# Kernel optimization log

Measured on AMD Instinct MI355X. Metric: run time of the kernel, lower is better.

Reference implementation:

```python
import jax, jax.numpy as jnp
import numpy as np

DIM = 768
HEADS = 12


def setup_inputs() -> dict:
    key = jax.random.key(0)
    ks = jax.random.split(key, 8)
    B, N, C = 4, 1024, DIM
    x = jax.random.normal(ks[0], (B, N, C), dtype=jnp.float32)
    mask = jax.random.normal(ks[1], (B, 1, N, N), dtype=jnp.float32)
    weight = jax.random.uniform(ks[2], (B, N), dtype=jnp.float32)
    s = 1.0 / np.sqrt(C)
    qkv_w = jax.random.normal(ks[3], (3 * C, C), dtype=jnp.float32) * s
    mu_w = jax.random.normal(ks[4], (C, C // 2), dtype=jnp.float32) * s
    mu_b = jnp.zeros((C,), dtype=jnp.float32)
    ls_w = jax.random.normal(ks[5], (C, C // 2), dtype=jnp.float32) * s
    ls_b = jnp.zeros((C,), dtype=jnp.float32)
    return {"x": x, "mask": mask, "weight": weight, "qkv_w": qkv_w,
            "mu_w": mu_w, "mu_b": mu_b, "ls_w": ls_w, "ls_b": ls_b}


def reference(x, mask, weight, qkv_w, mu_w, mu_b, ls_w, ls_b):
    B, N, C = x.shape
    H = HEADS
    Dh = C // H
    # NOTE: module uses head_dim = dim * num_heads for the scale (quirk, kept faithful)
    scale = (C * H) ** (-0.5)
    qkv = (x @ qkv_w.T).reshape(B, N, 3, H, Dh).transpose(2, 0, 3, 1, 4)  # [3,B,H,N,Dh]
    q, k, v = qkv[0], qkv[1], qkv[2]
    attn = jnp.einsum('bhnd,bhmd->bhnm', q, k) * scale + mask  # [B,H,N,N]
    attn = jax.nn.softmax(attn, axis=-1)
    # weight: [B,N] broadcast over heads and queries (key axis)
    w = weight[:, None, None, :] + 1e-10
    attn = attn * w
    attn = attn / attn.sum(axis=-1, keepdims=True)
    out = jnp.einsum('bhnm,bhmd->bhnd', attn, v)          # [B,H,N,Dh]
    out = out.transpose(0, 2, 1, 3).reshape(B, N, C)      # [B,N,C]
    mu_in = out[:, :, :C // 2]
    ls_in = out[:, :, C // 2:]
    mu = mu_in @ mu_w.T + mu_b
    logsigma = ls_in @ ls_w.T + ls_b
    return (mu, logsigma, attn)
```

## Files before the change

kernel.cpp:

```cpp
#include <hip/hip_runtime.h>
#include <hip/hip_bf16.h>

typedef __attribute__((ext_vector_type(8))) short short8;
typedef __attribute__((ext_vector_type(4))) float f32x4;
typedef __attribute__((ext_vector_type(4))) unsigned short u16x4;

#define NB 4
#define NN 1024
#define NC 768
#define NH 12
#define TC 2304

#define OFF_XB   0ul
#define OFF_WQ   6291456ul
#define OFF_WMU  (OFF_WQ + 3538944ul)
#define OFF_WLS  (OFF_WMU + 589824ul)
#define OFF_QKVB (OFF_WLS + 589824ul)
#define OFF_V3   (OFF_QKVB + 18874368ul)
#define OFF_OUTB (OFF_V3 + 6291456ul)

__device__ __forceinline__ unsigned short f2bf(float f) {
    unsigned int u = __float_as_uint(f);
    u = (u + 0x7FFFu + ((u >> 16) & 1u)) >> 16;
    return (unsigned short)u;
}

__device__ __forceinline__ void gload_lds16(const unsigned short* g, unsigned short* l) {
    __builtin_amdgcn_global_load_lds(
        (const __attribute__((address_space(1))) unsigned int*)g,
        (__attribute__((address_space(3))) unsigned int*)l, 16, 0, 0);
}

__device__ __forceinline__ void gload16(short8& dst, const unsigned short* p) {
    asm volatile("global_load_dwordx4 %0, %1, off" : "=v"(dst) : "v"(p));
}
__device__ __forceinline__ void gloadf4(f32x4& dst, const float* p) {
    asm volatile("global_load_dwordx4 %0, %1, off" : "=v"(dst) : "v"(p));
}
#define WAITV(N) do { asm volatile("s_waitcnt vmcnt(" #N ")" ::: "memory"); \
                      __builtin_amdgcn_sched_barrier(0); } while (0)
#define SBAR()   __builtin_amdgcn_sched_barrier(0)

__global__ void cast_all(const float* __restrict__ x, const float* __restrict__ qkv_w,
                         const float* __restrict__ mu_w, const float* __restrict__ ls_w,
                         unsigned short* __restrict__ dst) {
    int i = blockIdx.x * blockDim.x + threadIdx.x;
    const float* src; int off;
    if (i < 786432)            { src = x;     off = i; }
    else if (i < 1228800)      { src = qkv_w; off = i - 786432; }
    else if (i < 1302528)      { src = mu_w;  off = i - 1228800; }
    else                       { src = ls_w;  off = i - 1302528; }
    f32x4 v = ((const f32x4*)src)[off];
    u16x4 o;
#pragma unroll
    for (int j = 0; j < 4; ++j) o[j] = f2bf(v[j]);
    ((u16x4*)dst)[i] = o;
}

template <int EPI>
__device__ __forceinline__ void gemm_body(
    unsigned short* As, unsigned short* Bs,
    const unsigned short* __restrict__ A, const unsigned short* __restrict__ Bm,
    int K, int lda, int ldb, void* __restrict__ Cout, int ldc,
    const float* __restrict__ bias, int row0, int col0)
{
    const int t = threadIdx.x;
    const int lane = t & 63;
    const int wv = t >> 6;
    const int wm = wv >> 1, wn = wv & 1;
    const int li = lane & 15;
    const int koff = (lane >> 4) * 8;

    f32x4 acc[4][4] = {};

    const int tr = t >> 2;
    const int tc = (t & 3) * 8;
    const unsigned short* ag = A + (size_t)(row0 + tr) * lda + tc;
    const unsigned short* bg = Bm + (size_t)(col0 + tr) * ldb + tc;

    for (int kt = 0; kt < K; kt += 32) {
        gload_lds16(ag,            As + t * 8);
        gload_lds16(ag + 64 * lda, As + 2048 + t * 8);
        gload_lds16(bg,            Bs + t * 8);
        gload_lds16(bg + 64 * ldb, Bs + 2048 + t * 8);
        ag += 32; bg += 32;
        __syncthreads();
        short8 af[4], bf[4];
#pragma unroll
        for (int m = 0; m < 4; ++m)
            af[m] = *(const short8*)&As[(wm * 64 + m * 16 + li) * 32 + koff];
#pragma unroll
        for (int n = 0; n < 4; ++n)
            bf[n] = *(const short8*)&Bs[(wn * 64 + n * 16 + li) * 32 + koff];
#pragma unroll
        for (int m = 0; m < 4; ++m)
#pragma unroll
            for (int n = 0; n < 4; ++n)
                acc[m][n] = __builtin_amdgcn_mfma_f32_16x16x32_bf16(af[m], bf[n], acc[m][n], 0, 0, 0);
        __syncthreads();
    }

#pragma unroll
    for (int m = 0; m < 4; ++m) {
        const int row = row0 + wm * 64 + m * 16 + (lane >> 4) * 4;
#pragma unroll
        for (int n = 0; n < 4; ++n) {
            const int col = col0 + wn * 64 + n * 16 + li;
#pragma unroll
            for (int r = 0; r < 4; ++r) {
                if (EPI == 0) {
                    ((unsigned short*)Cout)[(size_t)(row + r) * ldc + col] = f2bf(acc[m][n][r]);
                } else {
                    ((float*)Cout)[(size_t)(row + r) * ldc + col] = acc[m][n][r] + bias[col];
                }
            }
        }
    }
}

__global__ __launch_bounds__(256, 2) void gemm_qkv(
    const unsigned short* __restrict__ A, const unsigned short* __restrict__ Bm,
    unsigned short* __restrict__ C)
{
    __shared__ unsigned short As[128 * 32];
    __shared__ unsigned short Bs[128 * 32];
    const int bid = blockIdx.y * gridDim.x + blockIdx.x;
    const int nwg = gridDim.x * gridDim.y;
    const int swz = (bid & 7) * (nwg >> 3) + (bid >> 3);
    const int row0 = (swz / gridDim.x) * 128;
    const int col0 = (swz % gridDim.x) * 128;
    gemm_body<0>(As, Bs, A, Bm, NC, NC, NC, C, TC, nullptr, row0, col0);
}

__global__ __launch_bounds__(256, 2) void gemm_heads(
    const unsigned short* __restrict__ outb,
    const unsigned short* __restrict__ wmu, const unsigned short* __restrict__ wls,
    const float* __restrict__ mu_b, const float* __restrict__ ls_b,
    float* __restrict__ out_mu, float* __restrict__ out_ls)
{
    __shared__ unsigned short As[128 * 32];
    __shared__ unsigned short Bs[128 * 32];
    const int bid = blockIdx.y * gridDim.x + blockIdx.x;
    const int nwg = gridDim.x * gridDim.y;
    const int swz = (bid & 7) * (nwg >> 3) + (bid >> 3);
    const int row0 = (swz / gridDim.x) * 128;
    const int col0 = (swz % gridDim.x) * 128;
    const int z = blockIdx.z;
    gemm_body<1>(As, Bs, outb + (z ? 384 : 0), z ? wls : wmu, 384, NC, 384,
                 z ? (void*)out_ls : (void*)out_mu, NC, z ? ls_b : mu_b, row0, col0);
}

__global__ __launch_bounds__(256, 4) void pack_kv(
    const unsigned short* __restrict__ qkvb, unsigned short* __restrict__ kp,
    unsigned short* __restrict__ v3)
{
    __shared__ unsigned short tile[64][65];
    const int t = threadIdx.x;
    const int bh = blockIdx.y;
    const int b = bh / NH, h = bh % NH;
    const int m0 = blockIdx.x * 64;
#pragma unroll
    for (int i = 0; i < 2; ++i) {
        int lin = i * 256 + t;
        int mr = lin >> 3;
        int dr = (lin & 7) * 8;
        short8 v = *(const short8*)(qkvb + (size_t)(b * NN + m0 + mr) * TC + 768 + h * 64 + dr);
        int dbyte = (dr * 2) ^ ((mr & 7) << 4);
        *(short8*)(kp + (size_t)(bh * NN + m0 + mr) * 64 + (dbyte >> 1)) = v;
    }
#pragma unroll
    for (int i = 0; i < 2; ++i) {
        int lin = i * 256 + t;
        int mr = lin >> 3;
        int dr = (lin & 7) * 8;
        short8 v = *(const short8*)(qkvb + (size_t)(b * NN + m0 + mr) * TC + 1536 + h * 64 + dr);
#pragma unroll
        for (int j = 0; j < 8; ++j) tile[mr][dr + j] = (unsigned short)v[j];
    }
    __syncthreads();
#pragma unroll
    for (int i = 0; i < 2; ++i) {
        int lin = i * 256 + t;
        int dw = lin >> 3;
        int mw = (lin & 7) * 8;
        short8 v;
#pragma unroll
        for (int j = 0; j < 8; ++j) v[j] = (short)tile[mw + j][dw];
        int kt = (m0 + mw) >> 5;
        int mm = mw & 31;
        *(short8*)(v3 + ((size_t)(bh * 32 + kt) * 64 + dw) * 32 + mm) = v;
    }
}

__global__ __launch_bounds__(256, 3) void attn_kernel(
    const unsigned short* __restrict__ qkvb, const unsigned short* __restrict__ kp,
    const unsigned short* __restrict__ v3, const float* __restrict__ mask,
    const float* __restrict__ weight, float* __restrict__ attn_out,
    unsigned short* __restrict__ outb)
{
    __shared__ char smem[33024];
    __shared__ float red_max[4][16];
    __shared__ float red_sum[4][16];

    const int t = threadIdx.x;
    const int lane = t & 63;
    const int wv = t >> 6;
    const int li = lane & 15;
    const int g = lane >> 4;
    const int koff = g * 8;
    const int bh = blockIdx.y;
    const int b = bh / NH, h = bh % NH;
    const int n0 = blockIdx.x * 16;
    const int cb = wv * 256;

    unsigned short* kw = (unsigned short*)smem + wv * 4096;
    const unsigned short* kps = kp + (size_t)bh * 65536 + cb * 64;
    const float* mrow = mask + (size_t)b * NN * NN + (size_t)(n0 + li) * NN + cb + g * 4;

    f32x4 w4;
    gloadf4(w4, weight + b * NN + cb + lane * 4);
    const unsigned short* qp = qkvb + (size_t)(b * NN + n0 + li) * TC + h * 64 + koff;
    short8 qf0, qf1;
    gload16(qf0, qp);
    gload16(qf1, qp + 32);

    f32x4 acc[16];
    f32x4 mk[2][2];

#define KISSUE(c) do {                                                        \
        const unsigned short* ks_ = kps + (c) * 2048;                         \
        unsigned short* kd_ = kw + ((c) & 1) * 2048;                          \
        gload_lds16(ks_ + 0 * 512 + lane * 8, kd_ + 0 * 512 + lane * 8);      \
        gload_lds16(ks_ + 1 * 512 + lane * 8, kd_ + 1 * 512 + lane * 8);      \
        gload_lds16(ks_ + 2 * 512 + lane * 8, kd_ + 2 * 512 + lane * 8);      \
        gload_lds16(ks_ + 3 * 512 + lane * 8, kd_ + 3 * 512 + lane * 8);      \
        gloadf4(mk[(c) & 1][0], mrow + ((c) * 2 + 0) * 16);                   \
        gloadf4(mk[(c) & 1][1], mrow + ((c) * 2 + 1) * 16);                   \
    } while (0)

#define KSTEP(c) do {                                                         \
        const unsigned short* kb_ = kw + ((c) & 1) * 2048;                    \
        const int swz_ = (li & 7) << 4;                                       \
        _Pragma("unroll")                                                     \
        for (int s = 0; s < 2; ++s) {                                         \
            const int keyb_ = (s * 16 + li) * 64;                             \
            short8 kf0 = *(const short8*)&kb_[keyb_ + (((g * 16) ^ swz_) >> 1)];        \
            short8 kf1 = *(const short8*)&kb_[keyb_ + (((64 + g * 16) ^ swz_) >> 1)];   \
            f32x4 ci = mk[(c) & 1][s] * 96.0f;                                \
            ci = __builtin_amdgcn_mfma_f32_16x16x32_bf16(kf0, qf0, ci, 0, 0, 0); \
            ci = __builtin_amdgcn_mfma_f32_16x16x32_bf16(kf1, qf1, ci, 0, 0, 0); \
            acc[(c) * 2 + s] = ci;                                            \
        }                                                                     \
    } while (0)

    KISSUE(0); KISSUE(1);
    WAITV(6);  KSTEP(0); SBAR(); KISSUE(2);
    WAITV(6);  KSTEP(1); SBAR(); KISSUE(3);
    WAITV(6);  KSTEP(2); SBAR(); KISSUE(4);
    WAITV(6);  KSTEP(3); SBAR(); KISSUE(5);
    WAITV(6);  KSTEP(4); SBAR(); KISSUE(6);
    WAITV(6);  KSTEP(5); SBAR(); KISSUE(7);
    WAITV(6);  KSTEP(6);
    WAITV(0);  KSTEP(7);
#undef KISSUE
#undef KSTEP

    const float scale = 1.0f / 96.0f;
    float rmax = -1e30f;
#pragma unroll
    for (int cf = 0; cf < 16; ++cf) {
#pragma unroll
        for (int r = 0; r < 4; ++r) rmax = fmaxf(rmax, acc[cf][r]);
    }
    rmax = fmaxf(rmax, __shfl_xor(rmax, 16, 64));
    rmax = fmaxf(rmax, __shfl_xor(rmax, 32, 64));
    if (lane < 16) red_max[wv][lane] = rmax;
    __syncthreads();
    rmax = fmaxf(fmaxf(red_max[0][li], red_max[1][li]),
                 fmaxf(red_max[2][li], red_max[3][li])) * scale;

    unsigned short (*P)[1032] = (unsigned short(*)[1032])smem;
    float rsum = 0.f;
#pragma unroll
    for (int cf = 0; cf < 16; ++cf) {
        f32x4 wcf;
#pragma unroll
        for (int r = 0; r < 4; ++r) wcf[r] = __shfl(w4[r], cf * 4 + g, 64);
        u16x4 pb;
#pragma unroll
        for (int r = 0; r < 4; ++r) {
            float p = __expf(acc[cf][r] * scale - rmax) * (wcf[r] + 1e-10f);
            acc[cf][r] = p;
            rsum += p;
            pb[r] = f2bf(p);
        }
        *(u16x4*)&P[li][cb + cf * 16 + g * 4] = pb;
    }
    rsum += __shfl_xor(rsum, 16, 64);
    rsum += __shfl_xor(rsum, 32, 64);
    if (lane < 16) red_sum[wv][lane] = rsum;
    __syncthreads();

    f32x4 o = {};
    const unsigned short* v3s = v3 + (size_t)bh * 65536 + wv * 512 + li * 32 + g * 8;
    short8 vA[8], vB[8];
#define VISSUE(c, vb2) do {                                                   \
        _Pragma("unroll")                                                     \
        for (int j = 0; j < 8; ++j) gload16(vb2[j], v3s + ((c) * 8 + j) * 2048); \
    } while (0)
#define VCOMP(c, vb2) do {                                                    \
        _Pragma("unroll")                                                     \
        for (int j = 0; j < 8; ++j) {                                         \
            short8 pa = *(const short8*)&P[li][((c) * 8 + j) * 32 + koff];    \
            o = __builtin_amdgcn_mfma_f32_16x16x32_bf16(pa, vb2[j], o, 0, 0, 0); \
        }                                                                     \
    } while (0)
    VISSUE(0, vA);
    VISSUE(1, vB);
    WAITV(8);  VCOMP(0, vA); SBAR(); VISSUE(2, vA);
    WAITV(8);  VCOMP(1, vB); SBAR(); VISSUE(3, vB);
    WAITV(8);  VCOMP(2, vA);
    WAITV(0);  VCOMP(3, vB);
#undef VISSUE
#undef VCOMP

    const float rinv = 1.0f / (red_sum[0][li] + red_sum[1][li]
                             + red_sum[2][li] + red_sum[3][li]);
    const int dcol = h * 64 + wv * 16 + li;
#pragma unroll
    for (int r = 0; r < 4; ++r) {
        const int row = g * 4 + r;
        const float rv = 1.0f / (red_sum[0][row] + red_sum[1][row]
                               + red_sum[2][row] + red_sum[3][row]);
        outb[(size_t)(b * NN + n0 + row) * NC + dcol] = f2bf(o[r] * rv);
    }

    float* arow = attn_out + (size_t)bh * NN * NN + (size_t)(n0 + li) * NN + cb + g * 4;
#pragma unroll
    for (int cf = 0; cf < 16; ++cf) {
        f32x4 a4;
#pragma unroll
        for (int r = 0; r < 4; ++r) a4[r] = acc[cf][r] * rinv;
        *(f32x4*)(arow + cf * 16) = a4;
    }
}

extern "C" void kernel_launch(void* const* d_in, const int* in_sizes, int n_in,
                              void* d_out, int out_size, void* d_ws, size_t ws_size,
                              hipStream_t stream) {
    const float* x      = (const float*)d_in[0];
    const float* mask   = (const float*)d_in[1];
    const float* weight = (const float*)d_in[2];
    const float* qkv_w  = (const float*)d_in[3];
    const float* mu_w   = (const float*)d_in[4];
    const float* mu_b   = (const float*)d_in[5];
    const float* ls_w   = (const float*)d_in[6];
    const float* ls_b   = (const float*)d_in[7];

    char* ws = (char*)d_ws;
    unsigned short* xb   = (unsigned short*)(ws + OFF_XB);
    unsigned short* kp   = (unsigned short*)(ws + OFF_XB);
    unsigned short* wq   = (unsigned short*)(ws + OFF_WQ);
    unsigned short* wmu  = (unsigned short*)(ws + OFF_WMU);
    unsigned short* wls  = (unsigned short*)(ws + OFF_WLS);
    unsigned short* qkvb = (unsigned short*)(ws + OFF_QKVB);
    unsigned short* v3   = (unsigned short*)(ws + OFF_V3);
    unsigned short* outb = (unsigned short*)(ws + OFF_OUTB);

    float* out_mu   = (float*)d_out;
    float* out_ls   = out_mu + 3145728;
    float* out_attn = out_mu + 6291456;

    cast_all<<<5376, 256, 0, stream>>>(x, qkv_w, mu_w, ls_w, xb);

    gemm_qkv<<<dim3(TC / 128, 4096 / 128), 256, 0, stream>>>(xb, wq, qkvb);

    pack_kv<<<dim3(NN / 64, NB * NH), 256, 0, stream>>>(qkvb, kp, v3);

    attn_kernel<<<dim3(NN / 16, NB * NH), 256, 0, stream>>>(
        qkvb, kp, v3, mask, weight, out_attn, outb);

    gemm_heads<<<dim3(NC / 128, 4096 / 128, 2), 256, 0, stream>>>(
        outb, wmu, wls, mu_b, ls_b, out_mu, out_ls);
}
```

Baseline: 161.5 us.

## Remap attention blocks per XCD for mask reuse and triple-buffer K tiles

Replaces the 2D grid with a 1D grid whose block index is decoded so that blocks on the same XCD share a (batch, query-tile) across all heads, letting the mask rows be reused in that XCD's L2. Also deepens the K/mask prefetch pipeline from double to triple buffering, raising LDS per block to 48KB and adding mask registers. This trades extra LDS and registers, which could hurt occupancy, for better memory latency hiding and cache hit rate.

```diff
diff --git a/kernel.cpp b/kernel.cpp
--- a/kernel.cpp
+++ b/kernel.cpp
@@ -198,7 +198,7 @@
     const float* __restrict__ weight, float* __restrict__ attn_out,
     unsigned short* __restrict__ outb)
 {
-    __shared__ char smem[33024];
+    __shared__ char smem[49152];
     __shared__ float red_max[4][16];
     __shared__ float red_sum[4][16];
 
@@ -208,12 +208,17 @@
     const int li = lane & 15;
     const int g = lane >> 4;
     const int koff = g * 8;
-    const int bh = blockIdx.y;
-    const int b = bh / NH, h = bh % NH;
-    const int n0 = blockIdx.x * 16;
+
+    const int bid = blockIdx.x;
+    const int xcd = bid & 7, slot = bid >> 3;
+    const int h = slot % 12, gh = slot / 12;
+    const int g12 = gh * 8 + xcd;
+    const int b = g12 >> 6, nt = g12 & 63;
+    const int n0 = nt * 16;
+    const int bh = b * NH + h;
     const int cb = wv * 256;
 
-    unsigned short* kw = (unsigned short*)smem + wv * 4096;
+    unsigned short* kw = (unsigned short*)smem + wv * 6144;
     const unsigned short* kps = kp + (size_t)bh * 65536 + cb * 64;
     const float* mrow = mask + (size_t)b * NN * NN + (size_t)(n0 + li) * NN + cb + g * 4;
 
@@ -225,42 +230,42 @@
     gload16(qf1, qp + 32);
 
     f32x4 acc[16];
-    f32x4 mk[2][2];
+    f32x4 mk[3][2];
 
 #define KISSUE(c) do {                                                        \
         const unsigned short* ks_ = kps + (c) * 2048;                         \
-        unsigned short* kd_ = kw + ((c) & 1) * 2048;                          \
+        unsigned short* kd_ = kw + ((c) % 3) * 2048;                          \
         gload_lds16(ks_ + 0 * 512 + lane * 8, kd_ + 0 * 512 + lane * 8);      \
         gload_lds16(ks_ + 1 * 512 + lane * 8, kd_ + 1 * 512 + lane * 8);      \
         gload_lds16(ks_ + 2 * 512 + lane * 8, kd_ + 2 * 512 + lane * 8);      \
         gload_lds16(ks_ + 3 * 512 + lane * 8, kd_ + 3 * 512 + lane * 8);      \
-        gloadf4(mk[(c) & 1][0], mrow + ((c) * 2 + 0) * 16);                   \
-        gloadf4(mk[(c) & 1][1], mrow + ((c) * 2 + 1) * 16);                   \
+        gloadf4(mk[(c) % 3][0], mrow + ((c) * 2 + 0) * 16);                   \
+        gloadf4(mk[(c) % 3][1], mrow + ((c) * 2 + 1) * 16);                   \
     } while (0)
 
 #define KSTEP(c) do {                                                         \
-        const unsigned short* kb_ = kw + ((c) & 1) * 2048;                    \
+        const unsigned short* kb_ = kw + ((c) % 3) * 2048;                    \
         const int swz_ = (li & 7) << 4;                                       \
         _Pragma("unroll")                                                     \
         for (int s = 0; s < 2; ++s) {                                         \
             const int keyb_ = (s * 16 + li) * 64;                             \
             short8 kf0 = *(const short8*)&kb_[keyb_ + (((g * 16) ^ swz_) >> 1)];        \
             short8 kf1 = *(const short8*)&kb_[keyb_ + (((64 + g * 16) ^ swz_) >> 1)];   \
-            f32x4 ci = mk[(c) & 1][s] * 96.0f;                                \
+            f32x4 ci = mk[(c) % 3][s] * 96.0f;                                \
             ci = __builtin_amdgcn_mfma_f32_16x16x32_bf16(kf0, qf0, ci, 0, 0, 0); \
             ci = __builtin_amdgcn_mfma_f32_16x16x32_bf16(kf1, qf1, ci, 0, 0, 0); \
             acc[(c) * 2 + s] = ci;                                            \
         }                                                                     \
     } while (0)
 
-    KISSUE(0); KISSUE(1);
-    WAITV(6);  KSTEP(0); SBAR(); KISSUE(2);
-    WAITV(6);  KSTEP(1); SBAR(); KISSUE(3);
-    WAITV(6);  KSTEP(2); SBAR(); KISSUE(4);
-    WAITV(6);  KSTEP(3); SBAR(); KISSUE(5);
-    WAITV(6);  KSTEP(4); SBAR(); KISSUE(6);
-    WAITV(6);  KSTEP(5); SBAR(); KISSUE(7);
-    WAITV(6);  KSTEP(6);
+    KISSUE(0); KISSUE(1); KISSUE(2);
+    WAITV(12); KSTEP(0); SBAR(); KISSUE(3);
+    WAITV(12); KSTEP(1); SBAR(); KISSUE(4);
+    WAITV(12); KSTEP(2); SBAR(); KISSUE(5);
+    WAITV(12); KSTEP(3); SBAR(); KISSUE(6);
+    WAITV(12); KSTEP(4); SBAR(); KISSUE(7);
+    WAITV(12); KSTEP(5); SBAR();
+    WAITV(6);  KSTEP(6); SBAR();
     WAITV(0);  KSTEP(7);
 #undef KISSUE
 #undef KSTEP
@@ -306,13 +311,13 @@
     short8 vA[8], vB[8];
 #define VISSUE(c, vb2) do {                                                   \
         _Pragma("unroll")                                                     \
-        for (int j = 0; j < 8; ++j) gload16(vb2[j], v3s + ((c) * 8 + j) * 2048); \
+        for (int j2 = 0; j2 < 8; ++j2) gload16(vb2[j2], v3s + ((c) * 8 + j2) * 2048); \
     } while (0)
 #define VCOMP(c, vb2) do {                                                    \
         _Pragma("unroll")                                                     \
-        for (int j = 0; j < 8; ++j) {                                         \
-            short8 pa = *(const short8*)&P[li][((c) * 8 + j) * 32 + koff];    \
-            o = __builtin_amdgcn_mfma_f32_16x16x32_bf16(pa, vb2[j], o, 0, 0, 0); \
+        for (int j2 = 0; j2 < 8; ++j2) {                                      \
+            short8 pa = *(const short8*)&P[li][((c) * 8 + j2) * 32 + koff];   \
+            o = __builtin_amdgcn_mfma_f32_16x16x32_bf16(pa, vb2[j2], o, 0, 0, 0); \
         }                                                                     \
     } while (0)
     VISSUE(0, vA);
@@ -377,7 +382,7 @@
 
     pack_kv<<<dim3(NN / 64, NB * NH), 256, 0, stream>>>(qkvb, kp, v3);
 
-    attn_kernel<<<dim3(NN / 16, NB * NH), 256, 0, stream>>>(
+    attn_kernel<<<3072, 256, 0, stream>>>(
         qkvb, kp, v3, mask, weight, out_attn, outb);
 
     gemm_heads<<<dim3(NC / 128, 4096 / 128, 2), 256, 0, stream>>>(
```

Measured after the change: 183.1 us. 1.13x slower.

## Split attention key range across 8 waves with split-K PV reduction

Applied to the files above, without the earlier changes.

Doubles the attention block to 512 threads so each wave handles 128 keys instead of 256, halving per-thread accumulators. The PV product is split in two across the key dimension, and the partial outputs are reduced through shared memory before normalization. Attention probability stores become nontemporal to avoid polluting cache with the large attn output. This adds an extra barrier and doubles LDS usage to 64KB per block, which may limit occupancy.

```diff
diff --git a/kernel.cpp b/kernel.cpp
--- a/kernel.cpp
+++ b/kernel.cpp
@@ -192,15 +192,16 @@
     }
 }
 
-__global__ __launch_bounds__(256, 3) void attn_kernel(
+__global__ __launch_bounds__(512, 4) void attn_kernel(
     const unsigned short* __restrict__ qkvb, const unsigned short* __restrict__ kp,
     const unsigned short* __restrict__ v3, const float* __restrict__ mask,
     const float* __restrict__ weight, float* __restrict__ attn_out,
     unsigned short* __restrict__ outb)
 {
-    __shared__ char smem[33024];
-    __shared__ float red_max[4][16];
-    __shared__ float red_sum[4][16];
+    __shared__ char smem[65536];
+    __shared__ float red_max[8][16];
+    __shared__ float red_sum[8][16];
+    __shared__ f32x4 po[4][64];
 
     const int t = threadIdx.x;
     const int lane = t & 63;
@@ -211,20 +212,20 @@
     const int bh = blockIdx.y;
     const int b = bh / NH, h = bh % NH;
     const int n0 = blockIdx.x * 16;
-    const int cb = wv * 256;
+    const int cb = wv * 128;
 
     unsigned short* kw = (unsigned short*)smem + wv * 4096;
     const unsigned short* kps = kp + (size_t)bh * 65536 + cb * 64;
     const float* mrow = mask + (size_t)b * NN * NN + (size_t)(n0 + li) * NN + cb + g * 4;
 
     f32x4 w4;
-    gloadf4(w4, weight + b * NN + cb + lane * 4);
+    gloadf4(w4, weight + b * NN + cb + (lane & 31) * 4);
     const unsigned short* qp = qkvb + (size_t)(b * NN + n0 + li) * TC + h * 64 + koff;
     short8 qf0, qf1;
     gload16(qf0, qp);
     gload16(qf1, qp + 32);
 
-    f32x4 acc[16];
+    f32x4 acc[8];
     f32x4 mk[2][2];
 
 #define KISSUE(c) do {                                                        \
@@ -256,19 +257,15 @@
     KISSUE(0); KISSUE(1);
     WAITV(6);  KSTEP(0); SBAR(); KISSUE(2);
     WAITV(6);  KSTEP(1); SBAR(); KISSUE(3);
-    WAITV(6);  KSTEP(2); SBAR(); KISSUE(4);
-    WAITV(6);  KSTEP(3); SBAR(); KISSUE(5);
-    WAITV(6);  KSTEP(4); SBAR(); KISSUE(6);
-    WAITV(6);  KSTEP(5); SBAR(); KISSUE(7);
-    WAITV(6);  KSTEP(6);
-    WAITV(0);  KSTEP(7);
+    WAITV(6);  KSTEP(2); SBAR();
+    WAITV(0);  KSTEP(3);
 #undef KISSUE
 #undef KSTEP
 
     const float scale = 1.0f / 96.0f;
     float rmax = -1e30f;
 #pragma unroll
-    for (int cf = 0; cf < 16; ++cf) {
+    for (int cf = 0; cf < 8; ++cf) {
 #pragma unroll
         for (int r = 0; r < 4; ++r) rmax = fmaxf(rmax, acc[cf][r]);
     }
@@ -276,13 +273,18 @@
     rmax = fmaxf(rmax, __shfl_xor(rmax, 32, 64));
     if (lane < 16) red_max[wv][lane] = rmax;
     __syncthreads();
-    rmax = fmaxf(fmaxf(red_max[0][li], red_max[1][li]),
-                 fmaxf(red_max[2][li], red_max[3][li])) * scale;
+    {
+        float m01 = fmaxf(red_max[0][li], red_max[1][li]);
+        float m23 = fmaxf(red_max[2][li], red_max[3][li]);
+        float m45 = fmaxf(red_max[4][li], red_max[5][li]);
+        float m67 = fmaxf(red_max[6][li], red_max[7][li]);
+        rmax = fmaxf(fmaxf(m01, m23), fmaxf(m45, m67)) * scale;
+    }
 
     unsigned short (*P)[1032] = (unsigned short(*)[1032])smem;
     float rsum = 0.f;
 #pragma unroll
-    for (int cf = 0; cf < 16; ++cf) {
+    for (int cf = 0; cf < 8; ++cf) {
         f32x4 wcf;
 #pragma unroll
         for (int r = 0; r < 4; ++r) wcf[r] = __shfl(w4[r], cf * 4 + g, 64);
@@ -301,47 +303,56 @@
     if (lane < 16) red_sum[wv][lane] = rsum;
     __syncthreads();
 
+    const int p4 = wv & 3, hf = wv >> 2;
     f32x4 o = {};
-    const unsigned short* v3s = v3 + (size_t)bh * 65536 + wv * 512 + li * 32 + g * 8;
-    short8 vA[8], vB[8];
+    const unsigned short* v3s = v3 + (size_t)bh * 65536 + (size_t)(hf * 16) * 2048
+                                  + p4 * 512 + li * 32 + g * 8;
+    short8 vA[4], vB[4];
 #define VISSUE(c, vb2) do {                                                   \
         _Pragma("unroll")                                                     \
-        for (int j = 0; j < 8; ++j) gload16(vb2[j], v3s + ((c) * 8 + j) * 2048); \
+        for (int j2 = 0; j2 < 4; ++j2) gload16(vb2[j2], v3s + ((c) * 4 + j2) * 2048); \
     } while (0)
 #define VCOMP(c, vb2) do {                                                    \
         _Pragma("unroll")                                                     \
-        for (int j = 0; j < 8; ++j) {                                         \
-            short8 pa = *(const short8*)&P[li][((c) * 8 + j) * 32 + koff];    \
-            o = __builtin_amdgcn_mfma_f32_16x16x32_bf16(pa, vb2[j], o, 0, 0, 0); \
+        for (int j2 = 0; j2 < 4; ++j2) {                                      \
+            short8 pa = *(const short8*)&P[li][(hf * 16 + (c) * 4 + j2) * 32 + koff]; \
+            o = __builtin_amdgcn_mfma_f32_16x16x32_bf16(pa, vb2[j2], o, 0, 0, 0); \
         }                                                                     \
     } while (0)
     VISSUE(0, vA);
     VISSUE(1, vB);
-    WAITV(8);  VCOMP(0, vA); SBAR(); VISSUE(2, vA);
-    WAITV(8);  VCOMP(1, vB); SBAR(); VISSUE(3, vB);
-    WAITV(8);  VCOMP(2, vA);
+    WAITV(4);  VCOMP(0, vA); SBAR(); VISSUE(2, vA);
+    WAITV(4);  VCOMP(1, vB); SBAR(); VISSUE(3, vB);
+    WAITV(4);  VCOMP(2, vA);
     WAITV(0);  VCOMP(3, vB);
 #undef VISSUE
 #undef VCOMP
 
-    const float rinv = 1.0f / (red_sum[0][li] + red_sum[1][li]
-                             + red_sum[2][li] + red_sum[3][li]);
-    const int dcol = h * 64 + wv * 16 + li;
-#pragma unroll
-    for (int r = 0; r < 4; ++r) {
-        const int row = g * 4 + r;
-        const float rv = 1.0f / (red_sum[0][row] + red_sum[1][row]
-                               + red_sum[2][row] + red_sum[3][row]);
-        outb[(size_t)(b * NN + n0 + row) * NC + dcol] = f2bf(o[r] * rv);
-    }
-
+    if (wv >= 4) po[p4][lane] = o;
+    __syncthreads();
+    if (wv < 4) {
+        f32x4 oo = po[p4][lane];
+        const int dcol = h * 64 + p4 * 16 + li;
+#pragma unroll
+        for (int r = 0; r < 4; ++r) {
+            const int row = g * 4 + r;
+            const float rs = red_sum[0][row] + red_sum[1][row] + red_sum[2][row]
+                           + red_sum[3][row] + red_sum[4][row] + red_sum[5][row]
+                           + red_sum[6][row] + red_sum[7][row];
+            outb[(size_t)(b * NN + n0 + row) * NC + dcol] = f2bf((o[r] + oo[r]) / rs);
+        }
+    }
+
+    const float rinv = 1.0f / (red_sum[0][li] + red_sum[1][li] + red_sum[2][li]
+                             + red_sum[3][li] + red_sum[4][li] + red_sum[5][li]
+                             + red_sum[6][li] + red_sum[7][li]);
     float* arow = attn_out + (size_t)bh * NN * NN + (size_t)(n0 + li) * NN + cb + g * 4;
 #pragma unroll
-    for (int cf = 0; cf < 16; ++cf) {
+    for (int cf = 0; cf < 8; ++cf) {
         f32x4 a4;
 #pragma unroll
         for (int r = 0; r < 4; ++r) a4[r] = acc[cf][r] * rinv;
-        *(f32x4*)(arow + cf * 16) = a4;
+        __builtin_nontemporal_store(a4, (f32x4*)(arow + cf * 16));
     }
 }
 
@@ -377,7 +388,7 @@
 
     pack_kv<<<dim3(NN / 64, NB * NH), 256, 0, stream>>>(qkvb, kp, v3);
 
-    attn_kernel<<<dim3(NN / 16, NB * NH), 256, 0, stream>>>(
+    attn_kernel<<<dim3(NN / 16, NB * NH), 512, 0, stream>>>(
         qkvb, kp, v3, mask, weight, out_attn, outb);
 
     gemm_heads<<<dim3(NC / 128, 4096 / 128, 2), 256, 0, stream>>>(
```

New measurement: 151.4 us. -6.2%, faster.
